# Performance work log

Hardware: AMD Instinct MI355X
Metric: run time of the kernel (lower is better)

Reference implementation:

```python
import jax, jax.numpy as jnp
import numpy as np

N_NODES = 50000
N_EDGES = 800000
IN_C, HID_C, OUT_C = 64, 128, 40


def setup_inputs() -> dict:
    key = jax.random.key(0)
    ks = jax.random.split(key, 8)
    x = jax.random.normal(ks[0], (N_NODES, IN_C), dtype=jnp.float32)
    edge_index = jax.random.randint(ks[1], (2, N_EDGES), 0, N_NODES, dtype=jnp.int64)
    def lin(k, fan_in, fan_out):
        # torch Linear default init: U(-1/sqrt(fan_in), 1/sqrt(fan_in))
        bound = 1.0 / np.sqrt(fan_in)
        kw, kb = jax.random.split(k)
        w = jax.random.uniform(kw, (fan_in, fan_out), minval=-bound, maxval=bound, dtype=jnp.float32)
        b = jax.random.uniform(kb, (fan_out,), minval=-bound, maxval=bound, dtype=jnp.float32)
        return w, b
    w1a, b1a = lin(ks[2], IN_C, HID_C)
    w1b, b1b = lin(ks[3], HID_C, HID_C)
    w2a, b2a = lin(ks[4], HID_C, HID_C)
    w2b, b2b = lin(ks[5], HID_C, OUT_C)
    return {
        'x': x, 'edge_index': edge_index,
        'w1a': w1a, 'b1a': b1a, 'w1b': w1b, 'b1b': b1b, 'eps1': jnp.float32(0.0),
        'w2a': w2a, 'b2a': b2a, 'w2b': w2b, 'b2b': b2b, 'eps2': jnp.float32(0.0),
    }


def _gin_conv(x, src, dst, eps, wa, ba, wb, bb):
    # aggregate: sum of neighbor (source) features at each destination node
    agg = jax.ops.segment_sum(x[src], dst, num_segments=N_NODES)  # [N, d]
    h = (1.0 + eps) * x + agg
    h = jax.nn.relu(h @ wa + ba)
    return h @ wb + bb


def reference(x, edge_index, w1a, b1a, w1b, b1b, eps1, w2a, b2a, w2b, b2b, eps2):
    src, dst = edge_index[0], edge_index[1]
    h = _gin_conv(x, src, dst, eps1, w1a, b1a, w1b, b1b)
    h = jax.nn.relu(h)
    # F.dropout(training=False) -> identity at inference
    h = _gin_conv(h, src, dst, eps2, w2a, b2a, w2b, b2b)
    return jax.nn.log_softmax(h, axis=1)
```

## Files before the change

### kernel.cpp

```cpp
#include <hip/hip_runtime.h>
#include <math.h>

#define N_NODES 50000
#define N_EDGES 800000
#define DUMMY   50000

typedef __attribute__((ext_vector_type(4))) _Float16 half4;
typedef __attribute__((ext_vector_type(8))) _Float16 half8;
typedef __attribute__((ext_vector_type(4))) float f32x4;

#define F_W1A 0
#define F_W1B (16 * 128)
#define F_W2A (48 * 128)
#define F_W2B (80 * 128)

__global__ __launch_bounds__(256) void prep(const float4* __restrict__ in,
    half4* __restrict__ xh4, int* __restrict__ zbase, half4* __restrict__ h1dummy,
    const float* __restrict__ w1a, const float* __restrict__ w1b,
    const float* __restrict__ w2a, const float* __restrict__ w2b,
    half8* __restrict__ wfrag)
{
    int i = blockIdx.x * 256 + threadIdx.x;
    if (i < 450000) zbase[i] = 0;
    if (i < 800000) {
        float4 v = in[i];
        half4 h;
        h[0] = (_Float16)v.x; h[1] = (_Float16)v.y;
        h[2] = (_Float16)v.z; h[3] = (_Float16)v.w;
        xh4[i] = h;
    } else if (i < 800016) {
        half4 zer = {(_Float16)0.f, (_Float16)0.f, (_Float16)0.f, (_Float16)0.f};
        xh4[i] = zer;
    }
    if (i < 32) {
        half4 zer = {(_Float16)0.f, (_Float16)0.f, (_Float16)0.f, (_Float16)0.f};
        h1dummy[i] = zer;
    }
    int j = i - 800032;
    if (j >= 0 && j < 5888) {
        int l = j & 63, f = j >> 6;
        const float* W; int fi, s, ct, Nw, base;
        if (f < 16)      { W = w1a; fi = f;      s = fi >> 3; ct = fi & 7;    Nw = 128; base = F_W1A; }
        else if (f < 48) { W = w1b; fi = f - 16; s = fi >> 3; ct = fi & 7;    Nw = 128; base = F_W1B; }
        else if (f < 80) { W = w2a; fi = f - 48; s = fi >> 3; ct = fi & 7;    Nw = 128; base = F_W2A; }
        else             { W = w2b; fi = f - 80; s = fi / 3;  ct = fi - s*3;  Nw = 40;  base = F_W2B; }
        int c = ct * 16 + (l & 15);
        int k0 = s * 32 + (l >> 4) * 8;
        half8 hi, lo;
        #pragma unroll
        for (int t = 0; t < 8; ++t) {
            float wv = (c < Nw) ? W[(k0 + t) * Nw + c] : 0.0f;
            _Float16 h = (_Float16)wv;
            hi[t] = h;
            lo[t] = (_Float16)(wv - (float)h);
        }
        wfrag[base + (fi * 2 + 0) * 64 + l] = hi;
        wfrag[base + (fi * 2 + 1) * 64 + l] = lo;
    }
}

__global__ __launch_bounds__(256) void scatter_ell(const int* __restrict__ src,
    const int* __restrict__ dst, int* __restrict__ cursor8, int* __restrict__ ovcur,
    unsigned short* __restrict__ ellp, unsigned short* __restrict__ ovell)
{
    int g = blockIdx.x & 7;
    int el = (blockIdx.x >> 3) * 256 + threadIdx.x;
    if (el >= 100000) return;
    int e = g * 100000 + el;
    int d = dst[e];
    unsigned short s = (unsigned short)src[e];
    int slot = atomicAdd(&cursor8[g * 50000 + d], 1);
    if (slot < 8) ellp[(size_t)(g * 50000 + d) * 8 + slot] = s;
    else {
        int o = atomicAdd(&ovcur[d], 1);
        if (o < 16) ovell[d * 16 + o] = s;
    }
}

__global__ __launch_bounds__(256) void gather64c(const half8* __restrict__ rows,
    const int* __restrict__ cursor8, const int* __restrict__ ovcur,
    const unsigned short* __restrict__ ellp, const unsigned short* __restrict__ ovell,
    unsigned short* __restrict__ ell, int* __restrict__ deg,
    const float* __restrict__ epsp, half8* __restrict__ z)
{
    __shared__ unsigned short buf[4][80];
    const float eps = 1.0f + epsp[0];
    const int lane = threadIdx.x & 63;
    const int w = threadIdx.x >> 6;
    const int q = lane & 7, p = lane >> 3;
    const int sl = lane & 7;
    const int wid = blockIdx.x * 4 + w;
    const int wstep = gridDim.x * 4;

    for (int node = wid; node < N_NODES; node += wstep) {
        int cg = min(cursor8[p * 50000 + node], 8);
        bool valid = sl < cg;
        unsigned short v = ellp[(size_t)(p * 50000 + node) * 8 + sl];
        unsigned long long mask = __ballot(valid);
        int total = __popcll(mask);
        int pos = __popcll(mask & ((1ULL << lane) - 1ULL));
        if (valid) buf[w][pos] = v;
        int ov = min(ovcur[node], 16);
        if (lane < ov) buf[w][total + lane] = ovell[node * 16 + lane];
        int tot = min(total + ov, 64);
        unsigned short e = (lane < tot) ? buf[w][lane] : (unsigned short)DUMMY;
        ell[((size_t)node << 6) + lane] = e;
        if (lane == 0) deg[node] = tot;
        int eidx = e;
        float acc[8];
        #pragma unroll
        for (int j = 0; j < 8; ++j) acc[j] = 0.f;
        for (int i = 0; i < tot; i += 32) {
            int s0 = __shfl(eidx, i + p);
            int s1 = __shfl(eidx, i + 8 + p);
            int s2 = __shfl(eidx, i + 16 + p);
            int s3 = __shfl(eidx, i + 24 + p);
            half8 v0 = rows[s0 * 8 + q];
            half8 v1 = rows[s1 * 8 + q];
            half8 v2 = rows[s2 * 8 + q];
            half8 v3 = rows[s3 * 8 + q];
            #pragma unroll
            for (int j = 0; j < 8; ++j)
                acc[j] += ((float)v0[j] + (float)v1[j]) + ((float)v2[j] + (float)v3[j]);
        }
        #pragma unroll
        for (int j = 0; j < 8; ++j) {
            acc[j] += __shfl_xor(acc[j], 8);
            acc[j] += __shfl_xor(acc[j], 16);
            acc[j] += __shfl_xor(acc[j], 32);
        }
        if (p == 0) {
            half8 sv = rows[node * 8 + q];
            half8 o;
            #pragma unroll
            for (int j = 0; j < 8; ++j) o[j] = (_Float16)fmaf(eps, (float)sv[j], acc[j]);
            z[node * 8 + q] = o;
        }
    }
}

__global__ __launch_bounds__(256) void gather128(const half8* __restrict__ rows,
    const unsigned short* __restrict__ ell, const int* __restrict__ deg,
    const float* __restrict__ epsp, half8* __restrict__ z)
{
    const float eps = 1.0f + epsp[0];
    const int lane = threadIdx.x & 63;
    const int q = lane & 15, p = lane >> 4;
    const int wid = blockIdx.x * 4 + (threadIdx.x >> 6);
    const int wstep = gridDim.x * 4;

    for (int node = wid; node < N_NODES; node += wstep) {
        const int cnt = deg[node];
        int eidx = ell[((size_t)node << 6) + lane];
        float acc[8];
        #pragma unroll
        for (int j = 0; j < 8; ++j) acc[j] = 0.f;
        for (int i = 0; i < cnt; i += 16) {
            int s0 = __shfl(eidx, i + p);
            int s1 = __shfl(eidx, i + 4 + p);
            int s2 = __shfl(eidx, i + 8 + p);
            int s3 = __shfl(eidx, i + 12 + p);
            half8 v0 = rows[s0 * 16 + q];
            half8 v1 = rows[s1 * 16 + q];
            half8 v2 = rows[s2 * 16 + q];
            half8 v3 = rows[s3 * 16 + q];
            #pragma unroll
            for (int j = 0; j < 8; ++j)
                acc[j] += ((float)v0[j] + (float)v1[j]) + ((float)v2[j] + (float)v3[j]);
        }
        #pragma unroll
        for (int j = 0; j < 8; ++j) {
            acc[j] += __shfl_xor(acc[j], 16);
            acc[j] += __shfl_xor(acc[j], 32);
        }
        if (p == 0) {
            half8 sv = rows[node * 16 + q];
            half8 o;
            #pragma unroll
            for (int j = 0; j < 8; ++j) o[j] = (_Float16)fmaf(eps, (float)sv[j], acc[j]);
            z[node * 16 + q] = o;
        }
    }
}

template<int KA, int NB, int EPI>
__global__ __launch_bounds__(256) void fused_mlp(const _Float16* __restrict__ A,
    const half8* __restrict__ wAF, const float* __restrict__ bA,
    const half8* __restrict__ wBF, const float* __restrict__ bB,
    void* __restrict__ Cout)
{
    constexpr int SA = KA / 32, CTB = NB / 16;
    __shared__ char mid[4][4096];
    const int tid = threadIdx.x;
    const int lane = tid & 63;
    const int wave = tid >> 6;
    const int gg = lane >> 4, r16 = lane & 15;
    const int tile = blockIdx.x * 4 + wave;
    if (tile >= (N_NODES + 15) / 16) return;
    char* my = mid[wave];

    const _Float16* Ar = A + (size_t)(tile * 16 + r16) * KA;
    f32x4 acc[8];
    #pragma unroll
    for (int ct = 0; ct < 8; ++ct) acc[ct] = (f32x4){0.f, 0.f, 0.f, 0.f};
    #pragma unroll
    for (int s = 0; s < SA; ++s) {
        half8 a = *(const half8*)(Ar + s * 32 + gg * 8);
        #pragma unroll
        for (int ct = 0; ct < 8; ++ct) {
            half8 bh = wAF[((s * 8 + ct) * 2 + 0) * 64 + lane];
            half8 bo = wAF[((s * 8 + ct) * 2 + 1) * 64 + lane];
            acc[ct] = __builtin_amdgcn_mfma_f32_16x16x32_f16(a, bh, acc[ct], 0, 0, 0);
            acc[ct] = __builtin_amdgcn_mfma_f32_16x16x32_f16(a, bo, acc[ct], 0, 0, 0);
        }
    }
    #pragma unroll
    for (int ct = 0; ct < 8; ++ct) {
        float bb = bA[ct * 16 + r16];
        #pragma unroll
        for (int r = 0; r < 4; ++r) {
            int row = gg * 4 + r;
            float v = fmaxf(acc[ct][r] + bb, 0.0f);
            int off = (row << 8) + ((ct * 16 + r16) << 1);
            off ^= (row & 7) << 4;
            *(_Float16*)(my + off) = (_Float16)v;
        }
    }

    half8 a2[4];
    #pragma unroll
    for (int s = 0; s < 4; ++s) {
        int off = (r16 << 8) + (s << 6) + (gg << 4);
        off ^= (r16 & 7) << 4;
        a2[s] = *(const half8*)(my + off);
    }
    f32x4 acc2[CTB];
    #pragma unroll
    for (int ct = 0; ct < CTB; ++ct) acc2[ct] = (f32x4){0.f, 0.f, 0.f, 0.f};
    #pragma unroll
    for (int s = 0; s < 4; ++s) {
        #pragma unroll
        for (int ct = 0; ct < CTB; ++ct) {
            half8 bh = wBF[((s * CTB + ct) * 2 + 0) * 64 + lane];
            half8 bo = wBF[((s * CTB + ct) * 2 + 1) * 64 + lane];
            acc2[ct] = __builtin_amdgcn_mfma_f32_16x16x32_f16(a2[s], bh, acc2[ct], 0, 0, 0);
            acc2[ct] = __builtin_amdgcn_mfma_f32_16x16x32_f16(a2[s], bo, acc2[ct], 0, 0, 0);
        }
    }

    if (EPI == 0) {
        _Float16* C = (_Float16*)Cout;
        #pragma unroll
        for (int ct = 0; ct < CTB; ++ct) {
            float bb = bB[ct * 16 + r16];
            #pragma unroll
            for (int r = 0; r < 4; ++r) {
                int row = tile * 16 + gg * 4 + r;
                float v = fmaxf(acc2[ct][r] + bb, 0.0f);
                C[(size_t)row * NB + ct * 16 + r16] = (_Float16)v;
            }
        }
    } else {
        float* C = (float*)Cout;
        const bool va2 = r16 < 8;
        float bl0 = bB[r16], bl1 = bB[16 + r16];
        float bl2 = va2 ? bB[32 + r16] : 0.0f;
        #pragma unroll
        for (int r = 0; r < 4; ++r) {
            int row = tile * 16 + gg * 4 + r;
            float v0 = acc2[0][r] + bl0;
            float v1 = acc2[1][r] + bl1;
            float v2 = acc2[2][r] + bl2;
            float mx = fmaxf(fmaxf(v0, v1), va2 ? v2 : -__builtin_inff());
            mx = fmaxf(mx, __shfl_xor(mx, 1));
            mx = fmaxf(mx, __shfl_xor(mx, 2));
            mx = fmaxf(mx, __shfl_xor(mx, 4));
            mx = fmaxf(mx, __shfl_xor(mx, 8));
            float sm = expf(v0 - mx) + expf(v1 - mx) + (va2 ? expf(v2 - mx) : 0.f);
            sm += __shfl_xor(sm, 1);
            sm += __shfl_xor(sm, 2);
            sm += __shfl_xor(sm, 4);
            sm += __shfl_xor(sm, 8);
            float ls = logf(sm) + mx;
            C[row * 40 + r16] = v0 - ls;
            C[row * 40 + 16 + r16] = v1 - ls;
            if (va2) C[row * 40 + 32 + r16] = v2 - ls;
        }
    }
}

extern "C" void kernel_launch(void* const* d_in, const int* in_sizes, int n_in,
                              void* d_out, int out_size, void* d_ws, size_t ws_size,
                              hipStream_t stream) {
    const float* x    = (const float*)d_in[0];
    const int*   ei   = (const int*)d_in[1];
    const float* w1a  = (const float*)d_in[2];
    const float* b1a  = (const float*)d_in[3];
    const float* w1b  = (const float*)d_in[4];
    const float* b1b  = (const float*)d_in[5];
    const float* eps1 = (const float*)d_in[6];
    const float* w2a  = (const float*)d_in[7];
    const float* b2a  = (const float*)d_in[8];
    const float* w2b  = (const float*)d_in[9];
    const float* b2b  = (const float*)d_in[10];
    const float* eps2 = (const float*)d_in[11];
    float* out = (float*)d_out;

    const int* srcIdx = ei;
    const int* dstIdx = ei + N_EDGES;

    char* ws = (char*)d_ws;
    int*            cursor8 = (int*)(ws);
    int*            ovcur   = (int*)(ws + 1600000);
    unsigned short* ellp    = (unsigned short*)(ws + 1800000);
    unsigned short* ovell   = (unsigned short*)(ws + 8200000);
    unsigned short* ell     = (unsigned short*)(ws + 9800000);
    int*            deg     = (int*)(ws + 16200000);
    half8*          wfrag   = (half8*)(ws + 16400000);
    _Float16*       xh      = (_Float16*)(ws + 16600000);
    _Float16*       z1h     = (_Float16*)(ws + 23000192);
    _Float16*       h1h     = (_Float16*)(ws + 29400192);
    _Float16*       z2h     = (_Float16*)(ws + 42200448);
    half4*          h1dummy = (half4*)(h1h + (size_t)DUMMY * 128);

    prep<<<3149, 256, 0, stream>>>((const float4*)x, (half4*)xh, cursor8, h1dummy,
                                   w1a, w1b, w2a, w2b, wfrag);
    scatter_ell<<<3128, 256, 0, stream>>>(srcIdx, dstIdx, cursor8, ovcur, ellp, ovell);

    gather64c<<<2048, 256, 0, stream>>>((const half8*)xh, cursor8, ovcur, ellp, ovell,
                                        ell, deg, eps1, (half8*)z1h);
    fused_mlp<64, 128, 0><<<782, 256, 0, stream>>>(z1h, wfrag + F_W1A, b1a,
                                                   wfrag + F_W1B, b1b, h1h);
    gather128<<<2048, 256, 0, stream>>>((const half8*)h1h, ell, deg, eps2, (half8*)z2h);
    fused_mlp<128, 48, 1><<<782, 256, 0, stream>>>(z2h, wfrag + F_W2A, b2a,
                                                   wfrag + F_W2B, b2b, out);
}
```

Measured before the change: 212.1 us.

## Merge prep and scatter, drop split-fp16 weights, recompute compacted neighbor lists

Merges the prep and scatter kernels into one launch with a block-range split, and moves zeroing of the counters to hipMemsetAsync. Weights are now stored as a single fp16 fragment with no hi/lo residual pair, which halves the MFMA work and weight loads in both MLPs but lowers weight precision. The compacted ELL/deg arrays are no longer written; the second gather recompacts neighbors from the per-group buckets instead. This removes a global write and read in exchange for repeating the compaction work. Scatter and prep now share one launch, but the scatter blocks still atomically update counters that the memset must have cleared first.

```diff
diff --git a/kernel.cpp b/kernel.cpp
--- a/kernel.cpp
+++ b/kernel.cpp
@@ -10,18 +10,38 @@
 typedef __attribute__((ext_vector_type(4))) float f32x4;
 
 #define F_W1A 0
-#define F_W1B (16 * 128)
-#define F_W2A (48 * 128)
-#define F_W2B (80 * 128)
-
-__global__ __launch_bounds__(256) void prep(const float4* __restrict__ in,
-    half4* __restrict__ xh4, int* __restrict__ zbase, half4* __restrict__ h1dummy,
+#define F_W1B (16 * 64)
+#define F_W2A (48 * 64)
+#define F_W2B (80 * 64)
+
+#define SCATTER_BLOCKS 3128
+#define PREP_BLOCKS    3149
+
+__global__ __launch_bounds__(256) void prep_scatter(
+    const int* __restrict__ src, const int* __restrict__ dst,
+    int* __restrict__ cursor8, int* __restrict__ ovcur,
+    unsigned short* __restrict__ ellp, unsigned short* __restrict__ ovell,
+    const float4* __restrict__ in, half4* __restrict__ xh4, half4* __restrict__ h1dummy,
     const float* __restrict__ w1a, const float* __restrict__ w1b,
     const float* __restrict__ w2a, const float* __restrict__ w2b,
     half8* __restrict__ wfrag)
 {
-    int i = blockIdx.x * 256 + threadIdx.x;
-    if (i < 450000) zbase[i] = 0;
+    if (blockIdx.x < SCATTER_BLOCKS) {
+        int g = blockIdx.x & 7;
+        int el = (blockIdx.x >> 3) * 256 + threadIdx.x;
+        if (el >= 100000) return;
+        int e = g * 100000 + el;
+        int d = dst[e];
+        unsigned short s = (unsigned short)src[e];
+        int slot = atomicAdd(&cursor8[g * 50000 + d], 1);
+        if (slot < 8) ellp[(size_t)(g * 50000 + d) * 8 + slot] = s;
+        else {
+            int o = atomicAdd(&ovcur[d], 1);
+            if (o < 16) ovell[d * 16 + o] = s;
+        }
+        return;
+    }
+    int i = (blockIdx.x - SCATTER_BLOCKS) * 256 + threadIdx.x;
     if (i < 800000) {
         float4 v = in[i];
         half4 h;
@@ -46,41 +66,39 @@
         else             { W = w2b; fi = f - 80; s = fi / 3;  ct = fi - s*3;  Nw = 40;  base = F_W2B; }
         int c = ct * 16 + (l & 15);
         int k0 = s * 32 + (l >> 4) * 8;
-        half8 hi, lo;
+        half8 hi;
         #pragma unroll
         for (int t = 0; t < 8; ++t) {
             float wv = (c < Nw) ? W[(k0 + t) * Nw + c] : 0.0f;
-            _Float16 h = (_Float16)wv;
-            hi[t] = h;
-            lo[t] = (_Float16)(wv - (float)h);
-        }
-        wfrag[base + (fi * 2 + 0) * 64 + l] = hi;
-        wfrag[base + (fi * 2 + 1) * 64 + l] = lo;
-    }
-}
-
-__global__ __launch_bounds__(256) void scatter_ell(const int* __restrict__ src,
-    const int* __restrict__ dst, int* __restrict__ cursor8, int* __restrict__ ovcur,
-    unsigned short* __restrict__ ellp, unsigned short* __restrict__ ovell)
-{
-    int g = blockIdx.x & 7;
-    int el = (blockIdx.x >> 3) * 256 + threadIdx.x;
-    if (el >= 100000) return;
-    int e = g * 100000 + el;
-    int d = dst[e];
-    unsigned short s = (unsigned short)src[e];
-    int slot = atomicAdd(&cursor8[g * 50000 + d], 1);
-    if (slot < 8) ellp[(size_t)(g * 50000 + d) * 8 + slot] = s;
-    else {
-        int o = atomicAdd(&ovcur[d], 1);
-        if (o < 16) ovell[d * 16 + o] = s;
-    }
+            hi[t] = (_Float16)wv;
+        }
+        wfrag[base + fi * 64 + l] = hi;
+    }
+}
+
+__device__ __forceinline__ int compact_nbrs(int node, int lane, int w,
+    const int* __restrict__ cursor8, const int* __restrict__ ovcur,
+    const unsigned short* __restrict__ ellp, const unsigned short* __restrict__ ovell,
+    unsigned short (*buf)[80], int* tot_out)
+{
+    const int gpl = lane >> 3, sl = lane & 7;
+    int cg = min(cursor8[gpl * 50000 + node], 8);
+    bool valid = sl < cg;
+    unsigned short v = ellp[(size_t)(gpl * 50000 + node) * 8 + sl];
+    unsigned long long mask = __ballot(valid);
+    int total = __popcll(mask);
+    int pos = __popcll(mask & ((1ULL << lane) - 1ULL));
+    if (valid) buf[w][pos] = v;
+    int ov = min(ovcur[node], 16);
+    if (lane < ov) buf[w][total + lane] = ovell[node * 16 + lane];
+    int tot = min(total + ov, 64);
+    *tot_out = tot;
+    return (lane < tot) ? (int)buf[w][lane] : DUMMY;
 }
 
 __global__ __launch_bounds__(256) void gather64c(const half8* __restrict__ rows,
     const int* __restrict__ cursor8, const int* __restrict__ ovcur,
     const unsigned short* __restrict__ ellp, const unsigned short* __restrict__ ovell,
-    unsigned short* __restrict__ ell, int* __restrict__ deg,
     const float* __restrict__ epsp, half8* __restrict__ z)
 {
     __shared__ unsigned short buf[4][80];
@@ -88,25 +106,12 @@
     const int lane = threadIdx.x & 63;
     const int w = threadIdx.x >> 6;
     const int q = lane & 7, p = lane >> 3;
-    const int sl = lane & 7;
     const int wid = blockIdx.x * 4 + w;
     const int wstep = gridDim.x * 4;
 
     for (int node = wid; node < N_NODES; node += wstep) {
-        int cg = min(cursor8[p * 50000 + node], 8);
-        bool valid = sl < cg;
-        unsigned short v = ellp[(size_t)(p * 50000 + node) * 8 + sl];
-        unsigned long long mask = __ballot(valid);
-        int total = __popcll(mask);
-        int pos = __popcll(mask & ((1ULL << lane) - 1ULL));
-        if (valid) buf[w][pos] = v;
-        int ov = min(ovcur[node], 16);
-        if (lane < ov) buf[w][total + lane] = ovell[node * 16 + lane];
-        int tot = min(total + ov, 64);
-        unsigned short e = (lane < tot) ? buf[w][lane] : (unsigned short)DUMMY;
-        ell[((size_t)node << 6) + lane] = e;
-        if (lane == 0) deg[node] = tot;
-        int eidx = e;
+        int tot;
+        int eidx = compact_nbrs(node, lane, w, cursor8, ovcur, ellp, ovell, buf, &tot);
         float acc[8];
         #pragma unroll
         for (int j = 0; j < 8; ++j) acc[j] = 0.f;
@@ -139,23 +144,26 @@
     }
 }
 
-__global__ __launch_bounds__(256) void gather128(const half8* __restrict__ rows,
-    const unsigned short* __restrict__ ell, const int* __restrict__ deg,
+__global__ __launch_bounds__(256) void gather128c(const half8* __restrict__ rows,
+    const int* __restrict__ cursor8, const int* __restrict__ ovcur,
+    const unsigned short* __restrict__ ellp, const unsigned short* __restrict__ ovell,
     const float* __restrict__ epsp, half8* __restrict__ z)
 {
+    __shared__ unsigned short buf[4][80];
     const float eps = 1.0f + epsp[0];
     const int lane = threadIdx.x & 63;
+    const int w = threadIdx.x >> 6;
     const int q = lane & 15, p = lane >> 4;
-    const int wid = blockIdx.x * 4 + (threadIdx.x >> 6);
+    const int wid = blockIdx.x * 4 + w;
     const int wstep = gridDim.x * 4;
 
     for (int node = wid; node < N_NODES; node += wstep) {
-        const int cnt = deg[node];
-        int eidx = ell[((size_t)node << 6) + lane];
+        int tot;
+        int eidx = compact_nbrs(node, lane, w, cursor8, ovcur, ellp, ovell, buf, &tot);
         float acc[8];
         #pragma unroll
         for (int j = 0; j < 8; ++j) acc[j] = 0.f;
-        for (int i = 0; i < cnt; i += 16) {
+        for (int i = 0; i < tot; i += 16) {
             int s0 = __shfl(eidx, i + p);
             int s1 = __shfl(eidx, i + 4 + p);
             int s2 = __shfl(eidx, i + 8 + p);
@@ -208,10 +216,8 @@
         half8 a = *(const half8*)(Ar + s * 32 + gg * 8);
         #pragma unroll
         for (int ct = 0; ct < 8; ++ct) {
-            half8 bh = wAF[((s * 8 + ct) * 2 + 0) * 64 + lane];
-            half8 bo = wAF[((s * 8 + ct) * 2 + 1) * 64 + lane];
+            half8 bh = wAF[(s * 8 + ct) * 64 + lane];
             acc[ct] = __builtin_amdgcn_mfma_f32_16x16x32_f16(a, bh, acc[ct], 0, 0, 0);
-            acc[ct] = __builtin_amdgcn_mfma_f32_16x16x32_f16(a, bo, acc[ct], 0, 0, 0);
         }
     }
     #pragma unroll
@@ -241,10 +247,8 @@
     for (int s = 0; s < 4; ++s) {
         #pragma unroll
         for (int ct = 0; ct < CTB; ++ct) {
-            half8 bh = wBF[((s * CTB + ct) * 2 + 0) * 64 + lane];
-            half8 bo = wBF[((s * CTB + ct) * 2 + 1) * 64 + lane];
+            half8 bh = wBF[(s * CTB + ct) * 64 + lane];
             acc2[ct] = __builtin_amdgcn_mfma_f32_16x16x32_f16(a2[s], bh, acc2[ct], 0, 0, 0);
-            acc2[ct] = __builtin_amdgcn_mfma_f32_16x16x32_f16(a2[s], bo, acc2[ct], 0, 0, 0);
         }
     }
 
@@ -314,24 +318,25 @@
     int*            ovcur   = (int*)(ws + 1600000);
     unsigned short* ellp    = (unsigned short*)(ws + 1800000);
     unsigned short* ovell   = (unsigned short*)(ws + 8200000);
-    unsigned short* ell     = (unsigned short*)(ws + 9800000);
-    int*            deg     = (int*)(ws + 16200000);
-    half8*          wfrag   = (half8*)(ws + 16400000);
-    _Float16*       xh      = (_Float16*)(ws + 16600000);
-    _Float16*       z1h     = (_Float16*)(ws + 23000192);
-    _Float16*       h1h     = (_Float16*)(ws + 29400192);
-    _Float16*       z2h     = (_Float16*)(ws + 42200448);
+    half8*          wfrag   = (half8*)(ws + 9800000);
+    _Float16*       xh      = (_Float16*)(ws + 9900000);
+    _Float16*       z1h     = (_Float16*)(ws + 16300160);
+    _Float16*       h1h     = (_Float16*)(ws + 22700160);
+    _Float16*       z2h     = (_Float16*)(ws + 35500416);
     half4*          h1dummy = (half4*)(h1h + (size_t)DUMMY * 128);
 
-    prep<<<3149, 256, 0, stream>>>((const float4*)x, (half4*)xh, cursor8, h1dummy,
-                                   w1a, w1b, w2a, w2b, wfrag);
-    scatter_ell<<<3128, 256, 0, stream>>>(srcIdx, dstIdx, cursor8, ovcur, ellp, ovell);
-
-    gather64c<<<2048, 256, 0, stream>>>((const half8*)xh, cursor8, ovcur, ellp, ovell,
-                                        ell, deg, eps1, (half8*)z1h);
+    hipMemsetAsync(cursor8, 0, 1800000, stream);
+
+    prep_scatter<<<SCATTER_BLOCKS + PREP_BLOCKS, 256, 0, stream>>>(
+        srcIdx, dstIdx, cursor8, ovcur, ellp, ovell,
+        (const float4*)x, (half4*)xh, h1dummy, w1a, w1b, w2a, w2b, wfrag);
+
+    gather64c<<<2048, 256, 0, stream>>>((const half8*)xh, cursor8, ovcur,
+                                        ellp, ovell, eps1, (half8*)z1h);
     fused_mlp<64, 128, 0><<<782, 256, 0, stream>>>(z1h, wfrag + F_W1A, b1a,
                                                    wfrag + F_W1B, b1b, h1h);
-    gather128<<<2048, 256, 0, stream>>>((const half8*)h1h, ell, deg, eps2, (half8*)z2h);
+    gather128c<<<2048, 256, 0, stream>>>((const half8*)h1h, cursor8, ovcur,
+                                         ellp, ovell, eps2, (half8*)z2h);
     fused_mlp<128, 48, 1><<<782, 256, 0, stream>>>(z2h, wfrag + F_W2A, b2a,
                                                    wfrag + F_W2B, b2b, out);
 }
```

After: 202.1 us. 4.7% less time.
